# Optimization experiments

Measured on AMD Instinct MI355X. Metric: run time of the kernel, lower is better.

The kernel has to match this reference:

```python
import jax, jax.numpy as jnp
import numpy as np

DIM = 1024
N_HEADS = 16
HEAD_DIM = DIM // N_HEADS


def setup_inputs() -> dict:
    key = jax.random.key(0)
    ks = jax.random.split(key, 7)
    B, S = 2, 2048
    scale = 0.02
    return {
        "q": jax.random.normal(ks[0], (B, S, DIM), dtype=jnp.float32),
        "k": jax.random.normal(ks[1], (B, S, DIM), dtype=jnp.float32),
        "v": jax.random.normal(ks[2], (B, S, DIM), dtype=jnp.float32),
        # torch nn.Linear weights are [out_features, in_features]; y = x @ W.T
        "wq": jax.random.normal(ks[3], (DIM, DIM), dtype=jnp.float32) * scale,
        "wk": jax.random.normal(ks[4], (DIM, DIM), dtype=jnp.float32) * scale,
        "wv": jax.random.normal(ks[5], (DIM, DIM), dtype=jnp.float32) * scale,
        "wo": jax.random.normal(ks[6], (DIM, DIM), dtype=jnp.float32) * scale,
    }


def reference(q, k, v, wq, wk, wv, wo):
    B, S, _ = q.shape
    H, D = N_HEADS, HEAD_DIM
    # projections (torch Linear: x @ W.T), reshape to [B, H, S, D]
    xq = (q @ wq.T).reshape(B, S, H, D).transpose(0, 2, 1, 3)
    xk = (k @ wk.T).reshape(B, S, H, D).transpose(0, 2, 1, 3)
    xv = (v @ wv.T).reshape(B, S, H, D).transpose(0, 2, 1, 3)
    # scaled dot-product attention with causal mask
    scores = jnp.einsum("bhqd,bhkd->bhqk", xq, xk) / jnp.sqrt(jnp.float32(D))
    causal = jnp.tril(jnp.ones((S, S), dtype=bool))
    scores = jnp.where(causal, scores, -jnp.inf)
    attn = jax.nn.softmax(scores.astype(jnp.float32), axis=-1).astype(xq.dtype)
    # dropout prob = 0.0 (eval-mode / deterministic reference)
    out = jnp.einsum("bhqk,bhkd->bhqd", attn, xv)
    out = out.transpose(0, 2, 1, 3).reshape(B, S, H * D)
    return out @ wo.T
```

## Files before the change

### kernel.cpp

```cpp
#include <hip/hip_runtime.h>
#include <hip/hip_bf16.h>
#include <stdint.h>


typedef short s16x8 __attribute__((ext_vector_type(8)));
typedef float f32x4 __attribute__((ext_vector_type(4)));

#define MFMA_BF16 __builtin_amdgcn_mfma_f32_16x16x32_bf16

static __device__ __forceinline__ unsigned short f2bf(float f) {
    union { float f; unsigned u; } x{f};
    unsigned r = x.u + 0x7fff + ((x.u >> 16) & 1);
    return (unsigned short)(r >> 16);
}
static __device__ __forceinline__ unsigned pk2(float a, float b) {
    return (unsigned)f2bf(a) | ((unsigned)f2bf(b) << 16);
}
static __device__ __forceinline__ unsigned pk2h(float a, float b) {
    __hip_bfloat162 h = __float22bfloat162_rn(float2{a, b});
    return *(unsigned*)&h;
}

static __device__ __forceinline__ void ald16(unsigned short* lds, const unsigned short* g) {
    __builtin_amdgcn_global_load_lds(
        (const __attribute__((address_space(1))) unsigned int*)g,
        (__attribute__((address_space(3))) unsigned int*)lds, 16, 0, 0);
}

#define QSCL 0.18033688f

__global__ __launch_bounds__(256) void convert_all_kernel(
        const float* __restrict__ q, const float* __restrict__ k,
        const float* __restrict__ v,
        const float* __restrict__ wq, const float* __restrict__ wk,
        const float* __restrict__ wv, const float* __restrict__ wo,
        unsigned short* __restrict__ dst) {
    const size_t idx = ((size_t)blockIdx.x * 256 + threadIdx.x) * 8;
    const int region = (int)(idx >> 22);
    const float* src;
    size_t off;
    if (region == 0)      { src = q; off = idx; }
    else if (region == 1) { src = k; off = idx & 4194303; }
    else if (region == 2) { src = v; off = idx & 4194303; }
    else {
        const int wsel = (int)((idx >> 20) & 3);
        src = wsel == 0 ? wq : wsel == 1 ? wk : wsel == 2 ? wv : wo;
        off = idx & 1048575;
    }
    const float4* p = (const float4*)(src + off);
    float4 a = p[0], b = p[1];
    uint4 u;
    u.x = pk2h(a.x, a.y); u.y = pk2h(a.z, a.w);
    u.z = pk2h(b.x, b.y); u.w = pk2h(b.z, b.w);
    *(uint4*)(dst + idx) = u;
}

__global__ __launch_bounds__(256) void wconvert_kernel(
        const float* __restrict__ wq, const float* __restrict__ wk,
        const float* __restrict__ wv, const float* __restrict__ wo,
        unsigned short* __restrict__ Wb) {
    const size_t idx = ((size_t)blockIdx.x * 256 + threadIdx.x) * 8;
    const int region = (int)(idx >> 20);
    const size_t off = idx & 1048575;
    const float* src = region == 0 ? wq : region == 1 ? wk : region == 2 ? wv : wo;
    const float4* p = (const float4*)(src + off);
    float4 a = p[0], b = p[1];
    uint4 u;
    u.x = pk2h(a.x, a.y); u.y = pk2h(a.z, a.w);
    u.z = pk2h(b.x, b.y); u.w = pk2h(b.z, b.w);
    *(uint4*)(Wb + idx) = u;
}

__global__ __launch_bounds__(256) void proj3b_kernel(
        const unsigned short* __restrict__ Qb, const unsigned short* __restrict__ Kb,
        const unsigned short* __restrict__ Vb, const unsigned short* __restrict__ Wb,
        unsigned short* __restrict__ Xq, unsigned short* __restrict__ Xk,
        unsigned short* __restrict__ Xvt) {
    constexpr int Kd = 1024;
    __shared__ union {
        struct { unsigned short A[128 * 32]; unsigned short B[128 * 32]; } s;
        unsigned short T[4 * 64 * 68];
    } sm;

    const int z = blockIdx.z;
    const unsigned short* A  = z == 0 ? Qb : z == 1 ? Kb : Vb;
    const unsigned short* Bw = Wb + (size_t)z * 1048576;

    const int t = threadIdx.x;
    const int m0 = blockIdx.x * 128, n0 = blockIdx.y * 128;
    const int w = t >> 6, lane = t & 63, fr = lane & 15, g = lane >> 4;
    const int wm = (w >> 1) * 64, wn = (w & 1) * 64;
    const int brow = t >> 2;
    const int cB = (t & 3) ^ ((t >> 3) & 3);
    const int sB = g ^ ((fr >> 1) & 3);

    f32x4 acc[4][4] = {};

    for (int k0 = 0; k0 < Kd; k0 += 32) {
        ald16(sm.s.A + (size_t)w * 512,        A  + (size_t)(m0 + brow) * Kd + k0 + cB * 8);
        ald16(sm.s.A + 2048 + (size_t)w * 512, A  + (size_t)(m0 + 64 + brow) * Kd + k0 + cB * 8);
        ald16(sm.s.B + (size_t)w * 512,        Bw + (size_t)(n0 + brow) * Kd + k0 + cB * 8);
        ald16(sm.s.B + 2048 + (size_t)w * 512, Bw + (size_t)(n0 + 64 + brow) * Kd + k0 + cB * 8);
        __syncthreads();

        s16x8 af[4], bfv[4];
#pragma unroll
        for (int mi = 0; mi < 4; ++mi)
            af[mi] = *(const s16x8*)(sm.s.A + (wm + mi * 16 + fr) * 32 + sB * 8);
#pragma unroll
        for (int ni = 0; ni < 4; ++ni)
            bfv[ni] = *(const s16x8*)(sm.s.B + (wn + ni * 16 + fr) * 32 + sB * 8);
#pragma unroll
        for (int mi = 0; mi < 4; ++mi)
#pragma unroll
            for (int ni = 0; ni < 4; ++ni)
                acc[mi][ni] = MFMA_BF16(af[mi], bfv[ni], acc[mi][ni], 0, 0, 0);
        __syncthreads();
    }

    if (z != 2) {
        unsigned short* C = z ? Xk : Xq;
        const float osc = z == 0 ? QSCL : 1.0f;
#pragma unroll
        for (int mi = 0; mi < 4; ++mi)
#pragma unroll
            for (int ni = 0; ni < 4; ++ni)
#pragma unroll
                for (int reg = 0; reg < 4; ++reg)
                    C[(size_t)(m0 + wm + mi * 16 + g * 4 + reg) * 1024 +
                      n0 + wn + ni * 16 + fr] = f2bf(acc[mi][ni][reg] * osc);
    } else {
        unsigned short* T = sm.T + w * (64 * 68);
#pragma unroll
        for (int mi = 0; mi < 4; ++mi)
#pragma unroll
            for (int ni = 0; ni < 4; ++ni) {
                uint2 u;
                u.x = pk2h(acc[mi][ni][0], acc[mi][ni][1]);
                u.y = pk2h(acc[mi][ni][2], acc[mi][ni][3]);
                *(uint2*)(T + (ni * 16 + fr) * 68 + mi * 16 + g * 4) = u;
            }
        __asm__ __volatile__("" ::: "memory");
#pragma unroll
        for (int pass = 0; pass < 8; ++pass) {
            const int row = pass * 8 + (lane >> 3);
            const int chk = lane & 7;
            uint4 d = *(const uint4*)(T + row * 68 + chk * 8);
            *(uint4*)(Xvt + (size_t)(n0 + wn + row) * 4096 + m0 + wm + chk * 8) = d;
        }
    }
}

__global__ __launch_bounds__(256) void proj3_kernel(
        const float* __restrict__ q, const float* __restrict__ k, const float* __restrict__ v,
        const unsigned short* __restrict__ Wb,
        unsigned short* __restrict__ Xq, unsigned short* __restrict__ Xk,
        unsigned short* __restrict__ Xvt) {
    constexpr int Kd = 1024;
    __shared__ unsigned short lsA[128 * 40];
    __shared__ unsigned short lsB[128 * 32];
    __shared__ unsigned short Tls[4 * 64 * 68];

    const int z = blockIdx.z;
    const float* A = z == 0 ? q : z == 1 ? k : v;
    const unsigned short* Bw = Wb + (size_t)z * 1048576;

    const int t = threadIdx.x;
    const int m0 = blockIdx.x * 128, n0 = blockIdx.y * 128;
    const int w = t >> 6, lane = t & 63, fr = lane & 15, g = lane >> 4, fq = g * 8;
    const int wm = (w >> 1) * 64, wn = (w & 1) * 64;
    const int ar = t >> 1, ac = (t & 1) * 16;
    const int brow = t >> 2;
    const int cB = (t & 3) ^ ((t >> 3) & 3);
    const int sB = g ^ ((fr >> 1) & 3);

    f32x4 acc[4][4] = {};

    for (int k0 = 0; k0 < Kd; k0 += 32) {
        ald16(lsB + (size_t)w * 512,        Bw + (size_t)(n0 + brow) * Kd + k0 + cB * 8);
        ald16(lsB + 2048 + (size_t)w * 512, Bw + (size_t)(n0 + 64 + brow) * Kd + k0 + cB * 8);
        {
            const float4* pa = (const float4*)(A + (size_t)(m0 + ar) * Kd + k0 + ac);
            float4 a0 = pa[0], a1 = pa[1], a2 = pa[2], a3 = pa[3];
            uint4 u0, u1;
            u0.x = pk2h(a0.x, a0.y); u0.y = pk2h(a0.z, a0.w);
            u0.z = pk2h(a1.x, a1.y); u0.w = pk2h(a1.z, a1.w);
            u1.x = pk2h(a2.x, a2.y); u1.y = pk2h(a2.z, a2.w);
            u1.z = pk2h(a3.x, a3.y); u1.w = pk2h(a3.z, a3.w);
            *(uint4*)(lsA + ar * 40 + ac)     = u0;
            *(uint4*)(lsA + ar * 40 + ac + 8) = u1;
        }
        __syncthreads();

        s16x8 af[4], bfv[4];
#pragma unroll
        for (int mi = 0; mi < 4; ++mi)
            af[mi] = *(const s16x8*)(lsA + (wm + mi * 16 + fr) * 40 + fq);
#pragma unroll
        for (int ni = 0; ni < 4; ++ni)
            bfv[ni] = *(const s16x8*)(lsB + (wn + ni * 16 + fr) * 32 + sB * 8);
#pragma unroll
        for (int mi = 0; mi < 4; ++mi)
#pragma unroll
            for (int ni = 0; ni < 4; ++ni)
                acc[mi][ni] = MFMA_BF16(af[mi], bfv[ni], acc[mi][ni], 0, 0, 0);
        __syncthreads();
    }

    if (z != 2) {
        unsigned short* C = z ? Xk : Xq;
        const float osc = z == 0 ? QSCL : 1.0f;
#pragma unroll
        for (int mi = 0; mi < 4; ++mi)
#pragma unroll
            for (int ni = 0; ni < 4; ++ni)
#pragma unroll
                for (int reg = 0; reg < 4; ++reg)
                    C[(size_t)(m0 + wm + mi * 16 + g * 4 + reg) * 1024 +
                      n0 + wn + ni * 16 + fr] = f2bf(acc[mi][ni][reg] * osc);
    } else {
        unsigned short* T = Tls + w * (64 * 68);
#pragma unroll
        for (int mi = 0; mi < 4; ++mi)
#pragma unroll
            for (int ni = 0; ni < 4; ++ni) {
                uint2 u;
                u.x = pk2h(acc[mi][ni][0], acc[mi][ni][1]);
                u.y = pk2h(acc[mi][ni][2], acc[mi][ni][3]);
                *(uint2*)(T + (ni * 16 + fr) * 68 + mi * 16 + g * 4) = u;
            }
        __asm__ __volatile__("" ::: "memory");
#pragma unroll
        for (int pass = 0; pass < 8; ++pass) {
            const int row = pass * 8 + (lane >> 3);
            const int chk = lane & 7;
            uint4 d = *(const uint4*)(T + row * 68 + chk * 8);
            *(uint4*)(Xvt + (size_t)(n0 + wn + row) * 4096 + m0 + wm + chk * 8) = d;
        }
    }
}

static __device__ __forceinline__ void slab_tail(
        const f32x4 sf[4], int kt, int qt, int qrow, float& l_part,
        f32x4* oacc, unsigned short* Pw, const s16x8 vf[4][2], int fr, int g) {
    float e[4][4];
    const bool diag = (kt == qt);
#pragma unroll
    for (int m16 = 0; m16 < 4; ++m16)
#pragma unroll
        for (int r = 0; r < 4; ++r) {
            float x = sf[m16][r];
            if (diag) {
                const int keyg = kt * 64 + m16 * 16 + g * 4 + r;
                x = (keyg <= qrow) ? x : -1e30f;
            }
            const float ee = exp2f(x);
            e[m16][r] = ee;
            l_part += ee;
        }
#pragma unroll
    for (int m16 = 0; m16 < 4; ++m16) {
        uint2 u;
        u.x = pk2h(e[m16][0], e[m16][1]);
        u.y = pk2h(e[m16][2], e[m16][3]);
        const int ch = 2 * m16 + (g >> 1);
        *(uint2*)(Pw + fr * 64 + ((ch ^ (fr & 7)) * 8) + (g & 1) * 4) = u;
    }
    __asm__ __volatile__("" ::: "memory");
    s16x8 pf0 = *(const s16x8*)(Pw + fr * 64 + ((g ^ (fr & 7)) * 8));
    s16x8 pf1 = *(const s16x8*)(Pw + fr * 64 + (((4 + g) ^ (fr & 7)) * 8));
#pragma unroll
    for (int m16 = 0; m16 < 4; ++m16) {
        oacc[m16] = MFMA_BF16(vf[m16][0], pf0, oacc[m16], 0, 0, 0);
        oacc[m16] = MFMA_BF16(vf[m16][1], pf1, oacc[m16], 0, 0, 0);
    }
}

__global__ __launch_bounds__(256, 2) void flash_attn_kernel(
        const unsigned short* __restrict__ Xq, const unsigned short* __restrict__ Xk,
        const unsigned short* __restrict__ Xvt, unsigned short* __restrict__ Oa) {
    __shared__ unsigned short Kls[64 * 64];
    __shared__ unsigned short Vls[64 * 64];
    __shared__ unsigned short Pls[2][4][16 * 64];

    const int t = threadIdx.x;
    const int bh = blockIdx.x;
    const int j = blockIdx.y;
    const int b = bh >> 4, h = bh & 15;
    const size_t rbase = (size_t)b * 2048;
    const int cbase = h * 64;

    const int w = t >> 6, lane = t & 63, fr = lane & 15, g = lane >> 4, fq = g * 8;
    const int qtH = 31 - j, qtL = j;
    const int qrowH = qtH * 64 + w * 16 + fr;
    const int qrowL = qtL * 64 + w * 16 + fr;

    const unsigned short* qpH = Xq + (rbase + qrowH) * 1024 + cbase;
    s16x8 qfH0 = *(const s16x8*)(qpH + fq);
    s16x8 qfH1 = *(const s16x8*)(qpH + 32 + fq);
    const unsigned short* qpL = Xq + (rbase + qrowL) * 1024 + cbase;
    s16x8 qfL0 = *(const s16x8*)(qpL + fq);
    s16x8 qfL1 = *(const s16x8*)(qpL + 32 + fq);

    float lH = 0.f, lL = 0.f;
    f32x4 oH[4] = {}, oL[4] = {};

    const int r0 = w * 16 + (lane >> 3), r1 = r0 + 8;
    const int s8 = lane & 7;
    const int c0 = s8 ^ (r0 & 7), c1 = s8 ^ (r1 & 7);

    for (int kt = 0; kt <= qtH; ++kt) {
        const unsigned short* ks = Xk + (rbase + kt * 64) * 1024 + cbase;
        ald16(Kls + (w * 16) * 64,     ks + (size_t)r0 * 1024 + c0 * 8);
        ald16(Kls + (w * 16 + 8) * 64, ks + (size_t)r1 * 1024 + c1 * 8);
        const unsigned short* vs = Xvt + rbase + kt * 64;
        ald16(Vls + (w * 16) * 64,     vs + (size_t)(cbase + r0) * 4096 + c0 * 8);
        ald16(Vls + (w * 16 + 8) * 64, vs + (size_t)(cbase + r1) * 4096 + c1 * 8);
        __syncthreads();

        const bool doL = (kt <= qtL);

        s16x8 kf[4][2], vf[4][2];
#pragma unroll
        for (int m16 = 0; m16 < 4; ++m16) {
            const int rr = m16 * 16 + fr;
            kf[m16][0] = *(const s16x8*)(Kls + rr * 64 + ((g ^ (fr & 7)) * 8));
            kf[m16][1] = *(const s16x8*)(Kls + rr * 64 + (((4 + g) ^ (fr & 7)) * 8));
            vf[m16][0] = *(const s16x8*)(Vls + rr * 64 + ((g ^ (fr & 7)) * 8));
            vf[m16][1] = *(const s16x8*)(Vls + rr * 64 + (((4 + g) ^ (fr & 7)) * 8));
        }

        f32x4 sH[4], sL[4];
#pragma unroll
        for (int m16 = 0; m16 < 4; ++m16) {
            f32x4 zz = {};
            zz = MFMA_BF16(kf[m16][0], qfH0, zz, 0, 0, 0);
            sH[m16] = MFMA_BF16(kf[m16][1], qfH1, zz, 0, 0, 0);
        }
        if (doL) {
#pragma unroll
            for (int m16 = 0; m16 < 4; ++m16) {
                f32x4 zz = {};
                zz = MFMA_BF16(kf[m16][0], qfL0, zz, 0, 0, 0);
                sL[m16] = MFMA_BF16(kf[m16][1], qfL1, zz, 0, 0, 0);
            }
        }
        slab_tail(sH, kt, qtH, qrowH, lH, oH, &Pls[0][w][0], vf, fr, g);
        if (doL)
            slab_tail(sL, kt, qtL, qrowL, lL, oL, &Pls[1][w][0], vf, fr, g);
        __syncthreads();
    }

    lH += __shfl_xor(lH, 16, 64);
    lH += __shfl_xor(lH, 32, 64);
    lL += __shfl_xor(lL, 16, 64);
    lL += __shfl_xor(lL, 32, 64);
    const float invH = 1.0f / lH, invL = 1.0f / lL;
#pragma unroll
    for (int m16 = 0; m16 < 4; ++m16) {
        uint2 u;
        u.x = pk2h(oH[m16][0] * invH, oH[m16][1] * invH);
        u.y = pk2h(oH[m16][2] * invH, oH[m16][3] * invH);
        *(uint2*)(Oa + (rbase + qrowH) * 1024 + cbase + m16 * 16 + g * 4) = u;
        uint2 u2;
        u2.x = pk2h(oL[m16][0] * invL, oL[m16][1] * invL);
        u2.y = pk2h(oL[m16][2] * invL, oL[m16][3] * invL);
        *(uint2*)(Oa + (rbase + qrowL) * 1024 + cbase + m16 * 16 + g * 4) = u2;
    }
}

__global__ __launch_bounds__(256) void outproj_kernel(
        const unsigned short* __restrict__ Oa, const unsigned short* __restrict__ Wo,
        float* __restrict__ out) {
    constexpr int Kd = 1024;
    __shared__ unsigned short lsA[64 * 32];
    __shared__ unsigned short lsB[128 * 32];

    const int t = threadIdx.x;
    const int m0 = blockIdx.x * 64, n0 = blockIdx.y * 128;
    const int w = t >> 6, lane = t & 63, fr = lane & 15, g = lane >> 4;
    const int wm = (w >> 1) * 32, wn = (w & 1) * 64;
    const int brow = t >> 2;
    const int cB = (t & 3) ^ ((t >> 3) & 3);
    const int sB = g ^ ((fr >> 1) & 3);

    f32x4 acc[2][4] = {};

    for (int k0 = 0; k0 < Kd; k0 += 32) {
        ald16(lsA + (size_t)w * 512,        Oa + (size_t)(m0 + brow) * Kd + k0 + cB * 8);
        ald16(lsB + (size_t)w * 512,        Wo + (size_t)(n0 + brow) * Kd + k0 + cB * 8);
        ald16(lsB + 2048 + (size_t)w * 512, Wo + (size_t)(n0 + 64 + brow) * Kd + k0 + cB * 8);
        __syncthreads();

        s16x8 af[2], bfv[4];
#pragma unroll
        for (int mi = 0; mi < 2; ++mi)
            af[mi] = *(const s16x8*)(lsA + (wm + mi * 16 + fr) * 32 + sB * 8);
#pragma unroll
        for (int ni = 0; ni < 4; ++ni)
            bfv[ni] = *(const s16x8*)(lsB + (wn + ni * 16 + fr) * 32 + sB * 8);
#pragma unroll
        for (int mi = 0; mi < 2; ++mi)
#pragma unroll
            for (int ni = 0; ni < 4; ++ni)
                acc[mi][ni] = MFMA_BF16(af[mi], bfv[ni], acc[mi][ni], 0, 0, 0);
        __syncthreads();
    }

#pragma unroll
    for (int mi = 0; mi < 2; ++mi)
#pragma unroll
        for (int ni = 0; ni < 4; ++ni)
#pragma unroll
            for (int reg = 0; reg < 4; ++reg)
                out[(size_t)(m0 + wm + mi * 16 + g * 4 + reg) * 1024 +
                    n0 + wn + ni * 16 + fr] = acc[mi][ni][reg];
}

extern "C" void kernel_launch(void* const* d_in, const int* in_sizes, int n_in,
                              void* d_out, int out_size, void* d_ws, size_t ws_size,
                              hipStream_t stream) {
    const float* q  = (const float*)d_in[0];
    const float* k  = (const float*)d_in[1];
    const float* v  = (const float*)d_in[2];
    const float* wq = (const float*)d_in[3];
    const float* wk = (const float*)d_in[4];
    const float* wv = (const float*)d_in[5];
    const float* wo = (const float*)d_in[6];
    float* out = (float*)d_out;

    if (ws_size >= (size_t)64 * 1024 * 1024) {
        unsigned short* base = (unsigned short*)d_ws;
        unsigned short* Qb  = base;
        unsigned short* Kb  = base + 4194304;
        unsigned short* Vb  = base + 8388608;
        unsigned short* Wb  = base + 12582912;
        unsigned short* Xq  = base + 16777216;
        unsigned short* Xk  = base + 20971520;
        unsigned short* Xvt = base + 25165824;
        unsigned short* Oa  = base + 29360128;

        convert_all_kernel<<<8192, 256, 0, stream>>>(q, k, v, wq, wk, wv, wo, base);
        proj3b_kernel<<<dim3(32, 8, 3), 256, 0, stream>>>(Qb, Kb, Vb, Wb, Xq, Xk, Xvt);
        flash_attn_kernel<<<dim3(32, 16), 256, 0, stream>>>(Xq, Xk, Xvt, Oa);
        outproj_kernel<<<dim3(64, 8), 256, 0, stream>>>(Oa, Wb + 3145728, out);
    } else {
        unsigned short* Wb  = (unsigned short*)d_ws;
        unsigned short* Xq  = Wb  + 4194304;
        unsigned short* Xk  = Xq  + 4194304;
        unsigned short* Xvt = Xk  + 4194304;
        unsigned short* Oa  = Xvt + 4194304;

        wconvert_kernel<<<2048, 256, 0, stream>>>(wq, wk, wv, wo, Wb);
        proj3_kernel<<<dim3(32, 8, 3), 256, 0, stream>>>(q, k, v, Wb, Xq, Xk, Xvt);
        flash_attn_kernel<<<dim3(32, 16), 256, 0, stream>>>(Xq, Xk, Xvt, Oa);
        outproj_kernel<<<dim3(64, 8), 256, 0, stream>>>(Oa, Wb + 3145728, out);
    }
}
```

Measured before the change: 220.1 us.

## Register-prefetch next K/V tile and share one P scratch buffer

```diff
diff --git a/kernel.cpp b/kernel.cpp
--- a/kernel.cpp
+++ b/kernel.cpp
@@ -12,9 +12,6 @@
     union { float f; unsigned u; } x{f};
     unsigned r = x.u + 0x7fff + ((x.u >> 16) & 1);
     return (unsigned short)(r >> 16);
-}
-static __device__ __forceinline__ unsigned pk2(float a, float b) {
-    return (unsigned)f2bf(a) | ((unsigned)f2bf(b) << 16);
 }
 static __device__ __forceinline__ unsigned pk2h(float a, float b) {
     __hip_bfloat162 h = __float22bfloat162_rn(float2{a, b});
@@ -274,6 +271,7 @@
         oacc[m16] = MFMA_BF16(vf[m16][0], pf0, oacc[m16], 0, 0, 0);
         oacc[m16] = MFMA_BF16(vf[m16][1], pf1, oacc[m16], 0, 0, 0);
     }
+    __asm__ __volatile__("" ::: "memory");
 }
 
 __global__ __launch_bounds__(256, 2) void flash_attn_kernel(
@@ -281,7 +279,7 @@
         const unsigned short* __restrict__ Xvt, unsigned short* __restrict__ Oa) {
     __shared__ unsigned short Kls[64 * 64];
     __shared__ unsigned short Vls[64 * 64];
-    __shared__ unsigned short Pls[2][4][16 * 64];
+    __shared__ unsigned short Pls[4][16 * 64];
 
     const int t = threadIdx.x;
     const int bh = blockIdx.x;
@@ -308,15 +306,30 @@
     const int r0 = w * 16 + (lane >> 3), r1 = r0 + 8;
     const int s8 = lane & 7;
     const int c0 = s8 ^ (r0 & 7), c1 = s8 ^ (r1 & 7);
+    const unsigned short* kbase = Xk + rbase * 1024 + cbase;
+    const size_t vrow0 = (size_t)(cbase + r0) * 4096 + rbase + c0 * 8;
+    const size_t vrow1 = (size_t)(cbase + r1) * 4096 + rbase + c1 * 8;
+
+    uint4 kA, kB, vA, vB;
+    kA = *(const uint4*)(kbase + (size_t)r0 * 1024 + c0 * 8);
+    kB = *(const uint4*)(kbase + (size_t)r1 * 1024 + c1 * 8);
+    vA = *(const uint4*)(Xvt + vrow0);
+    vB = *(const uint4*)(Xvt + vrow1);
 
     for (int kt = 0; kt <= qtH; ++kt) {
-        const unsigned short* ks = Xk + (rbase + kt * 64) * 1024 + cbase;
-        ald16(Kls + (w * 16) * 64,     ks + (size_t)r0 * 1024 + c0 * 8);
-        ald16(Kls + (w * 16 + 8) * 64, ks + (size_t)r1 * 1024 + c1 * 8);
-        const unsigned short* vs = Xvt + rbase + kt * 64;
-        ald16(Vls + (w * 16) * 64,     vs + (size_t)(cbase + r0) * 4096 + c0 * 8);
-        ald16(Vls + (w * 16 + 8) * 64, vs + (size_t)(cbase + r1) * 4096 + c1 * 8);
-        __syncthreads();
+        *(uint4*)(Kls + (w * 16) * 64 + lane * 8)     = kA;
+        *(uint4*)(Kls + (w * 16 + 8) * 64 + lane * 8) = kB;
+        *(uint4*)(Vls + (w * 16) * 64 + lane * 8)     = vA;
+        *(uint4*)(Vls + (w * 16 + 8) * 64 + lane * 8) = vB;
+        __syncthreads();
+
+        if (kt < qtH) {
+            const unsigned short* ks = kbase + (size_t)(kt + 1) * 65536;
+            kA = *(const uint4*)(ks + (size_t)r0 * 1024 + c0 * 8);
+            kB = *(const uint4*)(ks + (size_t)r1 * 1024 + c1 * 8);
+            vA = *(const uint4*)(Xvt + vrow0 + (size_t)(kt + 1) * 64);
+            vB = *(const uint4*)(Xvt + vrow1 + (size_t)(kt + 1) * 64);
+        }
 
         const bool doL = (kt <= qtL);
 
@@ -345,9 +358,9 @@
                 sL[m16] = MFMA_BF16(kf[m16][1], qfL1, zz, 0, 0, 0);
             }
         }
-        slab_tail(sH, kt, qtH, qrowH, lH, oH, &Pls[0][w][0], vf, fr, g);
+        slab_tail(sH, kt, qtH, qrowH, lH, oH, &Pls[w][0], vf, fr, g);
         if (doL)
-            slab_tail(sL, kt, qtL, qrowL, lL, oL, &Pls[1][w][0], vf, fr, g);
+            slab_tail(sL, kt, qtL, qrowL, lL, oL, &Pls[w][0], vf, fr, g);
         __syncthreads();
     }
 
```

New measurement: 213.6 us. -2.9%, faster.
